# Kernel optimization log

Hardware: AMD Instinct MI355X
Metric: run time of the kernel (lower is better)

## Reference

```python
import jax, jax.numpy as jnp
import numpy as np

B, V, NFEAT, INTER, NHID1, NHID12, NCLASS = 131072, 8, 32, 8, 16, 8, 2


def setup_inputs() -> dict:
    key = jax.random.key(0)
    ks = jax.random.split(key, 16)
    # node feature tensor: channel 0 = node type in {0,1}, channels 1..32 = features
    types = jax.random.randint(ks[0], (B, V, 1), 0, 2).astype(jnp.float32)
    feats = jax.random.normal(ks[1], (B, V, NFEAT), dtype=jnp.float32)
    x = jnp.concatenate([types, feats], axis=-1)  # (B, V, 33)
    adj = jax.random.uniform(ks[2], (B, V, V), dtype=jnp.float32)
    edge_attr = jax.random.normal(ks[3], (B, V, V), dtype=jnp.float32)
    s = lambda k, *sh: jax.random.normal(k, sh, dtype=jnp.float32) * 0.1
    return {
        "x": x, "adj": adj, "edge_attr": edge_attr,
        "wa": s(ks[4], INTER, NFEAT), "ba": jnp.zeros((INTER,), jnp.float32),
        "wb": s(ks[5], INTER, NFEAT), "bb": jnp.zeros((INTER,), jnp.float32),
        "w1": s(ks[6], NFEAT, NHID1), "b1": jnp.zeros((NHID1,), jnp.float32),
        "w2": s(ks[7], NHID1, NHID12), "b2": jnp.zeros((NHID12,), jnp.float32),
        "wg": s(ks[8], NHID12, NHID12), "bg": jnp.zeros((NHID12,), jnp.float32),
        "wf": s(ks[9], NCLASS, NHID12), "bf": jnp.zeros((NCLASS,), jnp.float32),
    }


def _attn_pool(h, wg, bg):
    # GlobalAttentionPooling: softmax(gate_nn(h)) over nodes, weighted sum
    gate = jax.nn.softmax(jnp.einsum('bvc,oc->bvo', h, wg) + bg, axis=1)
    return jnp.sum(gate * h, axis=1)  # (B, NHID12)


def reference(x, adj, edge_attr, wa, ba, wb, bb, w1, b1, w2, b2, wg, bg, wf, bf):
    node_types = x[..., 0]           # (B, V)
    feat = x[..., 1:]                # (B, V, 32)
    # conv_b (1x1 conv == per-node linear), output layout (B, inter, V)
    Fk = jnp.einsum('bvc,oc->bov', feat, wb) + bb[None, :, None]  # (B, 8, V=8)
    S = jax.nn.softmax(jnp.matmul(Fk, Fk), axis=1)                # (B, 8, 8)
    W = adj * (S + edge_attr)                                     # (B, V, V)
    # graph conv 1: (W @ feat) @ w1 + b1, LeakyReLU(0.01)
    h = jax.nn.leaky_relu(jnp.einsum('bvw,bwc->bvc', W, feat) @ w1 + b1)
    # graph conv 2
    h = jax.nn.leaky_relu(jnp.einsum('bvw,bwc->bvc', W, h) @ w2 + b2)  # (B, V, 8)
    # per-type masked attention pooling; types fixed to {0, 1}
    pooled = []
    for t in (0.0, 1.0):
        mask = (node_types == t)[..., None].astype(h.dtype)
        pooled.append(_attn_pool(h * mask, wg, bg))
    x_pool = jnp.mean(jnp.stack(pooled, axis=1), axis=1)  # (B, NHID12)
    return x_pool @ wf.T + bf  # (B, NCLASS)
```

## Files before the change

kernel.cpp:

```cpp
#include <hip/hip_runtime.h>


#define SLOTS 16
#define NTHREADS 128

typedef float v2f __attribute__((ext_vector_type(2)));
typedef float4 __attribute__((aligned(4))) f4u;

#define WBT 0
#define W1O 256
#define W2O 768
#define WGT 896
#define BBO 960
#define B1O 968
#define B2O 984
#define NWF 992

__device__ __forceinline__ float grp_sum8(float x) {
    x += __shfl_xor(x, 1);
    x += __shfl_xor(x, 2);
    x += __shfl_xor(x, 4);
    return x;
}
__device__ __forceinline__ void wavefence() { __builtin_amdgcn_wave_barrier(); }
__device__ __forceinline__ v2f mkv(float a, float b) { v2f r; r.x = a; r.y = b; return r; }

__global__ __launch_bounds__(NTHREADS, 4)
void gcn_fused(const float* __restrict__ x,
               const float* __restrict__ adj,
               const float* __restrict__ edge,
               const float* __restrict__ wb, const float* __restrict__ bb,
               const float* __restrict__ w1, const float* __restrict__ b1,
               const float* __restrict__ w2, const float* __restrict__ b2,
               const float* __restrict__ wg, const float* __restrict__ bg,
               const float* __restrict__ wf, const float* __restrict__ bf,
               float* __restrict__ out, int nGroups)
{
    __shared__ float lds[4096 + NWF];

    const int tid  = threadIdx.x;
    const int slot = tid >> 3;
    const int v    = tid & 7;
    const int sl   = slot & 7;
    const int wavebase = (slot >> 3) * 2048;
    float* xW = &lds[wavebase + sl * 256];
    float* A  = &lds[wavebase + sl * 72];
    float* Bg = &lds[wavebase + 576 + sl * 136];
    float* wS = &lds[4096];

    for (int i = tid; i < 256; i += NTHREADS) {
        const int o = i >> 5, c = i & 31;
        wS[WBT + c * 8 + o] = wb[i];
    }
    for (int i = tid; i < 512; i += NTHREADS) wS[W1O + i] = w1[i];
    if (tid < 128) wS[W2O + tid] = w2[tid];
    if (tid < 64) {
        const int o = tid >> 3, n = tid & 7;
        wS[WGT + n * 8 + o] = wg[tid];
    }
    if (tid < 8)  wS[BBO + tid] = bb[tid];
    if (tid < 16) wS[B1O + tid] = b1[tid];
    if (tid < 8)  wS[B2O + tid] = b2[tid];
    __syncthreads();

    long long bb_ = (long long)blockIdx.x * SLOTS + slot;
    if (bb_ >= (long long)nGroups * SLOTS) bb_ = (long long)nGroups * SLOTS - 1;
    const size_t b = (size_t)bb_;

    const float4* ar = (const float4*)(adj  + b * 64 + (size_t)v * 8);
    const float4* er = (const float4*)(edge + b * 64 + (size_t)v * 8);
    const float4 a0 = ar[0], a1 = ar[1];
    const float4 e0 = er[0], e1 = er[1];

    const float* xb = x + b * 264;
    const float type = xb[v * 33];
    float4 xf[8];
#pragma unroll
    for (int n = 0; n < 8; ++n)
        xf[n] = *(const f4u*)(xb + n * 33 + 1 + v * 4);

#pragma unroll
    for (int n = 0; n < 8; ++n)
        *(float4*)(xW + n * 32 + (((v + n + sl) & 7) << 2)) = xf[n];
    wavefence();

    const int K0 = (v + sl) & 7;

    v2f Fk2[4];
    {
        const v2f* bbp = (const v2f*)&wS[BBO];
#pragma unroll
        for (int p = 0; p < 4; ++p) Fk2[p] = bbp[p];
    }
    v2f g12[8];
#pragma unroll
    for (int p = 0; p < 8; ++p) g12[p] = mkv(0.f, 0.f);
#pragma unroll
    for (int k = 0; k < 8; ++k) {
        const float4 qk = *(const float4*)(xW + v * 32 + (((k + K0) & 7) << 2));
        const float f[4] = { qk.x, qk.y, qk.z, qk.w };
#pragma unroll
        for (int u = 0; u < 4; ++u) {
            const int c = 4 * k + u;
            const v2f f2 = mkv(f[u], f[u]);
            const float4* wbc = (const float4*)&wS[WBT + c * 8];
            const float4 wa = wbc[0], wbq = wbc[1];
            Fk2[0] = __builtin_elementwise_fma(f2, mkv(wa.x,  wa.y),  Fk2[0]);
            Fk2[1] = __builtin_elementwise_fma(f2, mkv(wa.z,  wa.w),  Fk2[1]);
            Fk2[2] = __builtin_elementwise_fma(f2, mkv(wbq.x, wbq.y), Fk2[2]);
            Fk2[3] = __builtin_elementwise_fma(f2, mkv(wbq.z, wbq.w), Fk2[3]);
            const float4* w1c = (const float4*)&wS[W1O + c * 16];
            const float4 wc0 = w1c[0], wc1 = w1c[1], wc2 = w1c[2], wc3 = w1c[3];
            g12[0] = __builtin_elementwise_fma(f2, mkv(wc0.x, wc0.y), g12[0]);
            g12[1] = __builtin_elementwise_fma(f2, mkv(wc0.z, wc0.w), g12[1]);
            g12[2] = __builtin_elementwise_fma(f2, mkv(wc1.x, wc1.y), g12[2]);
            g12[3] = __builtin_elementwise_fma(f2, mkv(wc1.z, wc1.w), g12[3]);
            g12[4] = __builtin_elementwise_fma(f2, mkv(wc2.x, wc2.y), g12[4]);
            g12[5] = __builtin_elementwise_fma(f2, mkv(wc2.z, wc2.w), g12[5]);
            g12[6] = __builtin_elementwise_fma(f2, mkv(wc3.x, wc3.y), g12[6]);
            g12[7] = __builtin_elementwise_fma(f2, mkv(wc3.z, wc3.w), g12[7]);
        }
    }
    wavefence();

#pragma unroll
    for (int p = 0; p < 4; ++p) {
        A[(2 * p)     * 8 + v] = Fk2[p].x;
        A[(2 * p + 1) * 8 + v] = Fk2[p].y;
    }
    {
        float4* gp = (float4*)(Bg + v * 16);
        gp[0] = make_float4(g12[0].x, g12[0].y, g12[1].x, g12[1].y);
        gp[1] = make_float4(g12[2].x, g12[2].y, g12[3].x, g12[3].y);
        gp[2] = make_float4(g12[4].x, g12[4].y, g12[5].x, g12[5].y);
        gp[3] = make_float4(g12[6].x, g12[6].y, g12[7].x, g12[7].y);
    }
    wavefence();

    float M[8];
#pragma unroll
    for (int o = 0; o < 8; ++o) {
        const float4* fr = (const float4*)(A + o * 8);
        const float4 r0 = fr[0], r1 = fr[1];
        v2f acc = mkv(0.f, 0.f);
        acc = __builtin_elementwise_fma(mkv(r0.x, r0.y), Fk2[0], acc);
        acc = __builtin_elementwise_fma(mkv(r0.z, r0.w), Fk2[1], acc);
        acc = __builtin_elementwise_fma(mkv(r1.x, r1.y), Fk2[2], acc);
        acc = __builtin_elementwise_fma(mkv(r1.z, r1.w), Fk2[3], acc);
        M[o] = acc.x + acc.y;
    }
    wavefence();
    float mx = M[0];
#pragma unroll
    for (int o = 1; o < 8; ++o) mx = fmaxf(mx, M[o]);
    float ssum = 0.f;
#pragma unroll
    for (int o = 0; o < 8; ++o) { M[o] = __expf(M[o] - mx); ssum += M[o]; }
    const float sinv = 1.f / ssum;
#pragma unroll
    for (int o = 0; o < 8; ++o) A[o * 8 + v] = M[o] * sinv;
    wavefence();

    const float4* sr = (const float4*)(A + v * 8);
    const float4 s0 = sr[0], s1 = sr[1];
    v2f W2[4];
    W2[0] = mkv(a0.x, a0.y) * (mkv(s0.x, s0.y) + mkv(e0.x, e0.y));
    W2[1] = mkv(a0.z, a0.w) * (mkv(s0.z, s0.w) + mkv(e0.z, e0.w));
    W2[2] = mkv(a1.x, a1.y) * (mkv(s1.x, s1.y) + mkv(e1.x, e1.y));
    W2[3] = mkv(a1.z, a1.w) * (mkv(s1.z, s1.w) + mkv(e1.z, e1.w));

    v2f m1[8];
#pragma unroll
    for (int p = 0; p < 8; ++p) m1[p] = mkv(0.f, 0.f);
#pragma unroll
    for (int w = 0; w < 8; ++w) {
        const float wv = (w & 1) ? W2[w >> 1].y : W2[w >> 1].x;
        const v2f f2 = mkv(wv, wv);
        const float4* gp = (const float4*)(Bg + w * 16);
        const float4 q0 = gp[0], q1 = gp[1], q2 = gp[2], q3 = gp[3];
        m1[0] = __builtin_elementwise_fma(f2, mkv(q0.x, q0.y), m1[0]);
        m1[1] = __builtin_elementwise_fma(f2, mkv(q0.z, q0.w), m1[1]);
        m1[2] = __builtin_elementwise_fma(f2, mkv(q1.x, q1.y), m1[2]);
        m1[3] = __builtin_elementwise_fma(f2, mkv(q1.z, q1.w), m1[3]);
        m1[4] = __builtin_elementwise_fma(f2, mkv(q2.x, q2.y), m1[4]);
        m1[5] = __builtin_elementwise_fma(f2, mkv(q2.z, q2.w), m1[5]);
        m1[6] = __builtin_elementwise_fma(f2, mkv(q3.x, q3.y), m1[6]);
        m1[7] = __builtin_elementwise_fma(f2, mkv(q3.z, q3.w), m1[7]);
    }
    v2f h[8];
    {
        const v2f* b1p = (const v2f*)&wS[B1O];
        const v2f k01 = mkv(0.01f, 0.01f);
#pragma unroll
        for (int p = 0; p < 8; ++p) {
            const v2f t = m1[p] + b1p[p];
            h[p] = __builtin_elementwise_max(t, t * k01);
        }
    }

    v2f g22[4];
#pragma unroll
    for (int p = 0; p < 4; ++p) g22[p] = mkv(0.f, 0.f);
#pragma unroll
    for (int j = 0; j < 16; ++j) {
        const float hv = (j & 1) ? h[j >> 1].y : h[j >> 1].x;
        const v2f f2 = mkv(hv, hv);
        const float4* w2r = (const float4*)&wS[W2O + j * 8];
        const float4 r0 = w2r[0], r1 = w2r[1];
        g22[0] = __builtin_elementwise_fma(f2, mkv(r0.x, r0.y), g22[0]);
        g22[1] = __builtin_elementwise_fma(f2, mkv(r0.z, r0.w), g22[1]);
        g22[2] = __builtin_elementwise_fma(f2, mkv(r1.x, r1.y), g22[2]);
        g22[3] = __builtin_elementwise_fma(f2, mkv(r1.z, r1.w), g22[3]);
    }
    wavefence();
    {
        float4* gp = (float4*)(A + v * 8);
        gp[0] = make_float4(g22[0].x, g22[0].y, g22[1].x, g22[1].y);
        gp[1] = make_float4(g22[2].x, g22[2].y, g22[3].x, g22[3].y);
    }
    wavefence();

    v2f m2[4];
#pragma unroll
    for (int p = 0; p < 4; ++p) m2[p] = mkv(0.f, 0.f);
#pragma unroll
    for (int w = 0; w < 8; ++w) {
        const float wv = (w & 1) ? W2[w >> 1].y : W2[w >> 1].x;
        const v2f f2 = mkv(wv, wv);
        const float4* gp = (const float4*)(A + w * 8);
        const float4 q0 = gp[0], q1 = gp[1];
        m2[0] = __builtin_elementwise_fma(f2, mkv(q0.x, q0.y), m2[0]);
        m2[1] = __builtin_elementwise_fma(f2, mkv(q0.z, q0.w), m2[1]);
        m2[2] = __builtin_elementwise_fma(f2, mkv(q1.x, q1.y), m2[2]);
        m2[3] = __builtin_elementwise_fma(f2, mkv(q1.z, q1.w), m2[3]);
    }
    v2f h2[4];
    {
        const v2f* b2p = (const v2f*)&wS[B2O];
        const v2f k01 = mkv(0.01f, 0.01f);
#pragma unroll
        for (int p = 0; p < 4; ++p) {
            const v2f t = m2[p] + b2p[p];
            h2[p] = __builtin_elementwise_max(t, t * k01);
        }
    }

    v2f Y2[4];
#pragma unroll
    for (int p = 0; p < 4; ++p) Y2[p] = mkv(0.f, 0.f);
#pragma unroll
    for (int n = 0; n < 8; ++n) {
        const float hv = (n & 1) ? h2[n >> 1].y : h2[n >> 1].x;
        const v2f f2 = mkv(hv, hv);
        const float4* wgr = (const float4*)&wS[WGT + n * 8];
        const float4 r0 = wgr[0], r1 = wgr[1];
        Y2[0] = __builtin_elementwise_fma(f2, mkv(r0.x, r0.y), Y2[0]);
        Y2[1] = __builtin_elementwise_fma(f2, mkv(r0.z, r0.w), Y2[1]);
        Y2[2] = __builtin_elementwise_fma(f2, mkv(r1.x, r1.y), Y2[2]);
        Y2[3] = __builtin_elementwise_fma(f2, mkv(r1.z, r1.w), Y2[3]);
    }
    wavefence();
    {
        float4* hp = (float4*)(A + v * 8);
        hp[0] = make_float4(h2[0].x, h2[0].y, h2[1].x, h2[1].y);
        hp[1] = make_float4(h2[2].x, h2[2].y, h2[3].x, h2[3].y);
        float4* yp = (float4*)(Bg + v * 8);
        yp[0] = make_float4(Y2[0].x, Y2[0].y, Y2[1].x, Y2[1].y);
        yp[1] = make_float4(Y2[2].x, Y2[2].y, Y2[3].x, Y2[3].y);
        Bg[64 + v] = type;
    }
    wavefence();

    const int o = v;
    float yc[8], hc[8], ty[8];
#pragma unroll
    for (int vp = 0; vp < 8; ++vp) {
        yc[vp] = Bg[vp * 8 + o];
        hc[vp] = A[vp * 8 + o];
        ty[vp] = Bg[64 + vp];
    }
    float xp = 0.f;
#pragma unroll
    for (int t = 0; t < 2; ++t) {
        const float tv = (float)t;
        float l[8];
        float lmx = -1e30f;
#pragma unroll
        for (int vp = 0; vp < 8; ++vp) {
            l[vp] = (ty[vp] == tv) ? yc[vp] : 0.f;
            lmx = fmaxf(lmx, l[vp]);
        }
        float esum = 0.f, num = 0.f;
#pragma unroll
        for (int vp = 0; vp < 8; ++vp) {
            const float e = __expf(l[vp] - lmx);
            esum += e;
            num  += (ty[vp] == tv) ? e * hc[vp] : 0.f;
        }
        xp += 0.5f * num / esum;
    }

    const float y0 = grp_sum8(xp * wf[0 * 8 + o]);
    const float y1 = grp_sum8(xp * wf[1 * 8 + o]);
    if (v == 0) {
        float2* op = (float2*)(out + b * 2);
        *op = make_float2(y0 + bf[0], y1 + bf[1]);
    }
}

extern "C" void kernel_launch(void* const* d_in, const int* in_sizes, int n_in,
                              void* d_out, int out_size, void* d_ws, size_t ws_size,
                              hipStream_t stream) {
    const float* x    = (const float*)d_in[0];
    const float* adj  = (const float*)d_in[1];
    const float* edge = (const float*)d_in[2];
    const float* wb   = (const float*)d_in[5];
    const float* bb   = (const float*)d_in[6];
    const float* w1   = (const float*)d_in[7];
    const float* b1   = (const float*)d_in[8];
    const float* w2   = (const float*)d_in[9];
    const float* b2   = (const float*)d_in[10];
    const float* wg   = (const float*)d_in[11];
    const float* bg   = (const float*)d_in[12];
    const float* wf   = (const float*)d_in[13];
    const float* bf   = (const float*)d_in[14];
    float* out = (float*)d_out;

    const int Btot    = in_sizes[0] / 264;
    const int nGroups = (Btot + SLOTS - 1) / SLOTS;

    gcn_fused<<<nGroups, NTHREADS, 0, stream>>>(x, adj, edge, wb, bb, w1, b1,
                                                w2, b2, wg, bg, wf, bf, out, nGroups);
}
```

Before: 271.3 us.

## Move weights to global workspace, shrink per-slot LDS, raise occupancy

A small prep kernel now packs the transposed weights into a global workspace, and the main kernel reads them from there instead of staging them in LDS behind a block-wide barrier. The per-slot LDS buffer shrinks by loading the 32 features in two halves and by splitting the 16-wide intermediate into two 8-wide passes. Together this cuts LDS from about 20 KB to about 9 KB per block, and launch bounds go from 4 to 6 to allow more blocks per CU. In exchange, weight reads go through global memory and cache instead of LDS, there is an extra kernel launch, and the split passes add wave barriers.

Result: slower. 302.5 us (+11.5%).

```diff
diff --git a/kernel.cpp b/kernel.cpp
--- a/kernel.cpp
+++ b/kernel.cpp
@@ -3,9 +3,6 @@
 
 #define SLOTS 16
 #define NTHREADS 128
-
-typedef float v2f __attribute__((ext_vector_type(2)));
-typedef float4 __attribute__((aligned(4))) f4u;
 
 #define WBT 0
 #define W1O 256
@@ -14,7 +11,12 @@
 #define BBO 960
 #define B1O 968
 #define B2O 984
-#define NWF 992
+#define WFO 992
+#define BFO 1008
+#define NWS 1010
+
+typedef float v2f __attribute__((ext_vector_type(2)));
+typedef float4 __attribute__((aligned(4))) f4u;
 
 __device__ __forceinline__ float grp_sum8(float x) {
     x += __shfl_xor(x, 1);
@@ -25,102 +27,114 @@
 __device__ __forceinline__ void wavefence() { __builtin_amdgcn_wave_barrier(); }
 __device__ __forceinline__ v2f mkv(float a, float b) { v2f r; r.x = a; r.y = b; return r; }
 
-__global__ __launch_bounds__(NTHREADS, 4)
+__global__ void gcn_prep(const float* __restrict__ wb, const float* __restrict__ bb,
+                         const float* __restrict__ w1, const float* __restrict__ b1,
+                         const float* __restrict__ w2, const float* __restrict__ b2,
+                         const float* __restrict__ wg, const float* __restrict__ wf,
+                         const float* __restrict__ bf, float* __restrict__ ws)
+{
+    const int t = threadIdx.x;
+    for (int i = t; i < 256; i += 256) ws[WBT + (i & 31) * 8 + (i >> 5)] = wb[i];
+    for (int i = t; i < 512; i += 256) ws[W1O + i] = w1[i];
+    if (t < 128) ws[W2O + t] = w2[t];
+    if (t < 64)  ws[WGT + (t & 7) * 8 + (t >> 3)] = wg[t];
+    if (t < 8)   ws[BBO + t] = bb[t];
+    if (t < 16)  ws[B1O + t] = b1[t];
+    if (t < 8)   ws[B2O + t] = b2[t];
+    if (t < 16)  ws[WFO + t] = wf[t];
+    if (t < 2)   ws[BFO + t] = bf[t];
+}
+
+
+#define KSTEP(kk, cb) { \
+    const float4 qk = *(const float4*)(SB + v * 16 + ((((kk) + 2 * sl + v) & 3) << 2)); \
+    const float f[4] = { qk.x, qk.y, qk.z, qk.w }; \
+    _Pragma("unroll") \
+    for (int u = 0; u < 4; ++u) { \
+        const int c = (cb) + u; \
+        const v2f f2 = mkv(f[u], f[u]); \
+        const float4* wbc = (const float4*)(wsW + WBT + c * 8); \
+        const float4 wa = wbc[0], wbq = wbc[1]; \
+        Fk2[0] = __builtin_elementwise_fma(f2, mkv(wa.x,  wa.y),  Fk2[0]); \
+        Fk2[1] = __builtin_elementwise_fma(f2, mkv(wa.z,  wa.w),  Fk2[1]); \
+        Fk2[2] = __builtin_elementwise_fma(f2, mkv(wbq.x, wbq.y), Fk2[2]); \
+        Fk2[3] = __builtin_elementwise_fma(f2, mkv(wbq.z, wbq.w), Fk2[3]); \
+        const float4* w1c = (const float4*)(wsW + W1O + c * 16); \
+        const float4 wc0 = w1c[0], wc1 = w1c[1], wc2 = w1c[2], wc3 = w1c[3]; \
+        g12[0] = __builtin_elementwise_fma(f2, mkv(wc0.x, wc0.y), g12[0]); \
+        g12[1] = __builtin_elementwise_fma(f2, mkv(wc0.z, wc0.w), g12[1]); \
+        g12[2] = __builtin_elementwise_fma(f2, mkv(wc1.x, wc1.y), g12[2]); \
+        g12[3] = __builtin_elementwise_fma(f2, mkv(wc1.z, wc1.w), g12[3]); \
+        g12[4] = __builtin_elementwise_fma(f2, mkv(wc2.x, wc2.y), g12[4]); \
+        g12[5] = __builtin_elementwise_fma(f2, mkv(wc2.z, wc2.w), g12[5]); \
+        g12[6] = __builtin_elementwise_fma(f2, mkv(wc3.x, wc3.y), g12[6]); \
+        g12[7] = __builtin_elementwise_fma(f2, mkv(wc3.z, wc3.w), g12[7]); \
+    } }
+
+__global__ __launch_bounds__(NTHREADS, 6)
 void gcn_fused(const float* __restrict__ x,
                const float* __restrict__ adj,
                const float* __restrict__ edge,
-               const float* __restrict__ wb, const float* __restrict__ bb,
-               const float* __restrict__ w1, const float* __restrict__ b1,
-               const float* __restrict__ w2, const float* __restrict__ b2,
-               const float* __restrict__ wg, const float* __restrict__ bg,
-               const float* __restrict__ wf, const float* __restrict__ bf,
+               const float* __restrict__ wsW,
                float* __restrict__ out, int nGroups)
 {
-    __shared__ float lds[4096 + NWF];
+    __shared__ __align__(16) float lds[2240];
 
     const int tid  = threadIdx.x;
     const int slot = tid >> 3;
     const int v    = tid & 7;
     const int sl   = slot & 7;
-    const int wavebase = (slot >> 3) * 2048;
-    float* xW = &lds[wavebase + sl * 256];
-    float* A  = &lds[wavebase + sl * 72];
-    float* Bg = &lds[wavebase + 576 + sl * 136];
-    float* wS = &lds[4096];
-
-    for (int i = tid; i < 256; i += NTHREADS) {
-        const int o = i >> 5, c = i & 31;
-        wS[WBT + c * 8 + o] = wb[i];
-    }
-    for (int i = tid; i < 512; i += NTHREADS) wS[W1O + i] = w1[i];
-    if (tid < 128) wS[W2O + tid] = w2[tid];
-    if (tid < 64) {
-        const int o = tid >> 3, n = tid & 7;
-        wS[WGT + n * 8 + o] = wg[tid];
-    }
-    if (tid < 8)  wS[BBO + tid] = bb[tid];
-    if (tid < 16) wS[B1O + tid] = b1[tid];
-    if (tid < 8)  wS[B2O + tid] = b2[tid];
-    __syncthreads();
+    float* SB = &lds[(slot >> 3) * 1120 + sl * 140];
+    float* A  = SB + 64;
 
     long long bb_ = (long long)blockIdx.x * SLOTS + slot;
     if (bb_ >= (long long)nGroups * SLOTS) bb_ = (long long)nGroups * SLOTS - 1;
     const size_t b = (size_t)bb_;
+
+    const float* xb = x + b * 264;
+    const int nb = v & 4;
+    const int cl = v & 3;
+    float4 xa[4];
+#pragma unroll
+    for (int i = 0; i < 4; ++i)
+        xa[i] = *(const f4u*)(xb + (nb + i) * 33 + 1 + cl * 4);
 
     const float4* ar = (const float4*)(adj  + b * 64 + (size_t)v * 8);
     const float4* er = (const float4*)(edge + b * 64 + (size_t)v * 8);
     const float4 a0 = ar[0], a1 = ar[1];
     const float4 e0 = er[0], e1 = er[1];
-
-    const float* xb = x + b * 264;
     const float type = xb[v * 33];
-    float4 xf[8];
-#pragma unroll
-    for (int n = 0; n < 8; ++n)
-        xf[n] = *(const f4u*)(xb + n * 33 + 1 + v * 4);
-
-#pragma unroll
-    for (int n = 0; n < 8; ++n)
-        *(float4*)(xW + n * 32 + (((v + n + sl) & 7) << 2)) = xf[n];
-    wavefence();
-
-    const int K0 = (v + sl) & 7;
+
+#pragma unroll
+    for (int i = 0; i < 4; ++i) {
+        const int n = nb + i;
+        *(float4*)(SB + n * 16 + (((cl + 2 * sl + n) & 3) << 2)) = xa[i];
+    }
+    float4 xc[4];
+#pragma unroll
+    for (int i = 0; i < 4; ++i)
+        xc[i] = *(const f4u*)(xb + (nb + i) * 33 + 17 + cl * 4);
+    wavefence();
 
     v2f Fk2[4];
     {
-        const v2f* bbp = (const v2f*)&wS[BBO];
+        const v2f* bbp = (const v2f*)&wsW[BBO];
 #pragma unroll
         for (int p = 0; p < 4; ++p) Fk2[p] = bbp[p];
     }
     v2f g12[8];
 #pragma unroll
     for (int p = 0; p < 8; ++p) g12[p] = mkv(0.f, 0.f);
-#pragma unroll
-    for (int k = 0; k < 8; ++k) {
-        const float4 qk = *(const float4*)(xW + v * 32 + (((k + K0) & 7) << 2));
-        const float f[4] = { qk.x, qk.y, qk.z, qk.w };
-#pragma unroll
-        for (int u = 0; u < 4; ++u) {
-            const int c = 4 * k + u;
-            const v2f f2 = mkv(f[u], f[u]);
-            const float4* wbc = (const float4*)&wS[WBT + c * 8];
-            const float4 wa = wbc[0], wbq = wbc[1];
-            Fk2[0] = __builtin_elementwise_fma(f2, mkv(wa.x,  wa.y),  Fk2[0]);
-            Fk2[1] = __builtin_elementwise_fma(f2, mkv(wa.z,  wa.w),  Fk2[1]);
-            Fk2[2] = __builtin_elementwise_fma(f2, mkv(wbq.x, wbq.y), Fk2[2]);
-            Fk2[3] = __builtin_elementwise_fma(f2, mkv(wbq.z, wbq.w), Fk2[3]);
-            const float4* w1c = (const float4*)&wS[W1O + c * 16];
-            const float4 wc0 = w1c[0], wc1 = w1c[1], wc2 = w1c[2], wc3 = w1c[3];
-            g12[0] = __builtin_elementwise_fma(f2, mkv(wc0.x, wc0.y), g12[0]);
-            g12[1] = __builtin_elementwise_fma(f2, mkv(wc0.z, wc0.w), g12[1]);
-            g12[2] = __builtin_elementwise_fma(f2, mkv(wc1.x, wc1.y), g12[2]);
-            g12[3] = __builtin_elementwise_fma(f2, mkv(wc1.z, wc1.w), g12[3]);
-            g12[4] = __builtin_elementwise_fma(f2, mkv(wc2.x, wc2.y), g12[4]);
-            g12[5] = __builtin_elementwise_fma(f2, mkv(wc2.z, wc2.w), g12[5]);
-            g12[6] = __builtin_elementwise_fma(f2, mkv(wc3.x, wc3.y), g12[6]);
-            g12[7] = __builtin_elementwise_fma(f2, mkv(wc3.z, wc3.w), g12[7]);
-        }
-    }
+
+    KSTEP(0, 0) KSTEP(1, 4) KSTEP(2, 8) KSTEP(3, 12)
+    wavefence();
+#pragma unroll
+    for (int i = 0; i < 4; ++i) {
+        const int n = nb + i;
+        *(float4*)(SB + n * 16 + (((cl + 2 * sl + n) & 3) << 2)) = xc[i];
+    }
+    wavefence();
+    KSTEP(0, 16) KSTEP(1, 20) KSTEP(2, 24) KSTEP(3, 28)
     wavefence();
 
 #pragma unroll
@@ -129,11 +143,9 @@
         A[(2 * p + 1) * 8 + v] = Fk2[p].y;
     }
     {
-        float4* gp = (float4*)(Bg + v * 16);
+        float4* gp = (float4*)(SB + v * 8);
         gp[0] = make_float4(g12[0].x, g12[0].y, g12[1].x, g12[1].y);
         gp[1] = make_float4(g12[2].x, g12[2].y, g12[3].x, g12[3].y);
-        gp[2] = make_float4(g12[4].x, g12[4].y, g12[5].x, g12[5].y);
-        gp[3] = make_float4(g12[6].x, g12[6].y, g12[7].x, g12[7].y);
     }
     wavefence();
 
@@ -176,20 +188,34 @@
     for (int w = 0; w < 8; ++w) {
         const float wv = (w & 1) ? W2[w >> 1].y : W2[w >> 1].x;
         const v2f f2 = mkv(wv, wv);
-        const float4* gp = (const float4*)(Bg + w * 16);
-        const float4 q0 = gp[0], q1 = gp[1], q2 = gp[2], q3 = gp[3];
+        const float4* gp = (const float4*)(SB + w * 8);
+        const float4 q0 = gp[0], q1 = gp[1];
         m1[0] = __builtin_elementwise_fma(f2, mkv(q0.x, q0.y), m1[0]);
         m1[1] = __builtin_elementwise_fma(f2, mkv(q0.z, q0.w), m1[1]);
         m1[2] = __builtin_elementwise_fma(f2, mkv(q1.x, q1.y), m1[2]);
         m1[3] = __builtin_elementwise_fma(f2, mkv(q1.z, q1.w), m1[3]);
-        m1[4] = __builtin_elementwise_fma(f2, mkv(q2.x, q2.y), m1[4]);
-        m1[5] = __builtin_elementwise_fma(f2, mkv(q2.z, q2.w), m1[5]);
-        m1[6] = __builtin_elementwise_fma(f2, mkv(q3.x, q3.y), m1[6]);
-        m1[7] = __builtin_elementwise_fma(f2, mkv(q3.z, q3.w), m1[7]);
+    }
+    wavefence();
+    {
+        float4* gp = (float4*)(SB + v * 8);
+        gp[0] = make_float4(g12[4].x, g12[4].y, g12[5].x, g12[5].y);
+        gp[1] = make_float4(g12[6].x, g12[6].y, g12[7].x, g12[7].y);
+    }
+    wavefence();
+#pragma unroll
+    for (int w = 0; w < 8; ++w) {
+        const float wv = (w & 1) ? W2[w >> 1].y : W2[w >> 1].x;
+        const v2f f2 = mkv(wv, wv);
+        const float4* gp = (const float4*)(SB + w * 8);
+        const float4 q0 = gp[0], q1 = gp[1];
+        m1[4] = __builtin_elementwise_fma(f2, mkv(q0.x, q0.y), m1[4]);
+        m1[5] = __builtin_elementwise_fma(f2, mkv(q0.z, q0.w), m1[5]);
+        m1[6] = __builtin_elementwise_fma(f2, mkv(q1.x, q1.y), m1[6]);
+        m1[7] = __builtin_elementwise_fma(f2, mkv(q1.z, q1.w), m1[7]);
     }
     v2f h[8];
     {
-        const v2f* b1p = (const v2f*)&wS[B1O];
+        const v2f* b1p = (const v2f*)&wsW[B1O];
         const v2f k01 = mkv(0.01f, 0.01f);
 #pragma unroll
         for (int p = 0; p < 8; ++p) {
@@ -205,7 +231,7 @@
     for (int j = 0; j < 16; ++j) {
         const float hv = (j & 1) ? h[j >> 1].y : h[j >> 1].x;
         const v2f f2 = mkv(hv, hv);
-        const float4* w2r = (const float4*)&wS[W2O + j * 8];
+        const float4* w2r = (const float4*)(wsW + W2O + j * 8);
         const float4 r0 = w2r[0], r1 = w2r[1];
         g22[0] = __builtin_elementwise_fma(f2, mkv(r0.x, r0.y), g22[0]);
         g22[1] = __builtin_elementwise_fma(f2, mkv(r0.z, r0.w), g22[1]);
@@ -214,7 +240,7 @@
     }
     wavefence();
     {
-        float4* gp = (float4*)(A + v * 8);
+        float4* gp = (float4*)(SB + v * 8);
         gp[0] = make_float4(g22[0].x, g22[0].y, g22[1].x, g22[1].y);
         gp[1] = make_float4(g22[2].x, g22[2].y, g22[3].x, g22[3].y);
     }
@@ -227,7 +253,7 @@
     for (int w = 0; w < 8; ++w) {
         const float wv = (w & 1) ? W2[w >> 1].y : W2[w >> 1].x;
         const v2f f2 = mkv(wv, wv);
-        const float4* gp = (const float4*)(A + w * 8);
+        const float4* gp = (const float4*)(SB + w * 8);
         const float4 q0 = gp[0], q1 = gp[1];
         m2[0] = __builtin_elementwise_fma(f2, mkv(q0.x, q0.y), m2[0]);
         m2[1] = __builtin_elementwise_fma(f2, mkv(q0.z, q0.w), m2[1]);
@@ -236,7 +262,7 @@
     }
     v2f h2[4];
     {
-        const v2f* b2p = (const v2f*)&wS[B2O];
+        const v2f* b2p = (const v2f*)&wsW[B2O];
         const v2f k01 = mkv(0.01f, 0.01f);
 #pragma unroll
         for (int p = 0; p < 4; ++p) {
@@ -252,7 +278,7 @@
     for (int n = 0; n < 8; ++n) {
         const float hv = (n & 1) ? h2[n >> 1].y : h2[n >> 1].x;
         const v2f f2 = mkv(hv, hv);
-        const float4* wgr = (const float4*)&wS[WGT + n * 8];
+        const float4* wgr = (const float4*)(wsW + WGT + n * 8);
         const float4 r0 = wgr[0], r1 = wgr[1];
         Y2[0] = __builtin_elementwise_fma(f2, mkv(r0.x, r0.y), Y2[0]);
         Y2[1] = __builtin_elementwise_fma(f2, mkv(r0.z, r0.w), Y2[1]);
@@ -261,13 +287,12 @@
     }
     wavefence();
     {
-        float4* hp = (float4*)(A + v * 8);
-        hp[0] = make_float4(h2[0].x, h2[0].y, h2[1].x, h2[1].y);
-        hp[1] = make_float4(h2[2].x, h2[2].y, h2[3].x, h2[3].y);
-        float4* yp = (float4*)(Bg + v * 8);
-        yp[0] = make_float4(Y2[0].x, Y2[0].y, Y2[1].x, Y2[1].y);
-        yp[1] = make_float4(Y2[2].x, Y2[2].y, Y2[3].x, Y2[3].y);
-        Bg[64 + v] = type;
+        float4* pp = (float4*)(SB + v * 16);
+        pp[0] = make_float4(Y2[0].x, h2[0].x, Y2[0].y, h2[0].y);
+        pp[1] = make_float4(Y2[1].x, h2[1].x, Y2[1].y, h2[1].y);
+        pp[2] = make_float4(Y2[2].x, h2[2].x, Y2[2].y, h2[2].y);
+        pp[3] = make_float4(Y2[3].x, h2[3].x, Y2[3].y, h2[3].y);
+        SB[128 + v] = type;
     }
     wavefence();
 
@@ -275,9 +300,10 @@
     float yc[8], hc[8], ty[8];
 #pragma unroll
     for (int vp = 0; vp < 8; ++vp) {
-        yc[vp] = Bg[vp * 8 + o];
-        hc[vp] = A[vp * 8 + o];
-        ty[vp] = Bg[64 + vp];
+        const float2 q = *(const float2*)(SB + vp * 16 + o * 2);
+        yc[vp] = q.x;
+        hc[vp] = q.y;
+        ty[vp] = SB[128 + vp];
     }
     float xp = 0.f;
 #pragma unroll
@@ -300,11 +326,11 @@
         xp += 0.5f * num / esum;
     }
 
-    const float y0 = grp_sum8(xp * wf[0 * 8 + o]);
-    const float y1 = grp_sum8(xp * wf[1 * 8 + o]);
+    const float y0 = grp_sum8(xp * wsW[WFO + o]);
+    const float y1 = grp_sum8(xp * wsW[WFO + 8 + o]);
     if (v == 0) {
         float2* op = (float2*)(out + b * 2);
-        *op = make_float2(y0 + bf[0], y1 + bf[1]);
+        *op = make_float2(y0 + wsW[BFO], y1 + wsW[BFO + 1]);
     }
 }
 
@@ -321,14 +347,14 @@
     const float* w2   = (const float*)d_in[9];
     const float* b2   = (const float*)d_in[10];
     const float* wg   = (const float*)d_in[11];
-    const float* bg   = (const float*)d_in[12];
     const float* wf   = (const float*)d_in[13];
     const float* bf   = (const float*)d_in[14];
     float* out = (float*)d_out;
+    float* ws  = (float*)d_ws;
 
     const int Btot    = in_sizes[0] / 264;
     const int nGroups = (Btot + SLOTS - 1) / SLOTS;
 
-    gcn_fused<<<nGroups, NTHREADS, 0, stream>>>(x, adj, edge, wb, bb, w1, b1,
-                                                w2, b2, wg, bg, wf, bf, out, nGroups);
+    gcn_prep<<<1, 256, 0, stream>>>(wb, bb, w1, b1, w2, b2, wg, wf, bf, ws);
+    gcn_fused<<<nGroups, NTHREADS, 0, stream>>>(x, adj, edge, ws, out, nGroups);
 }
```
